# Kernel tuning notes

Measured on AMD Instinct MI355X. Metric: run time of the kernel, lower is better.

Reference implementation:

```python
import jax, jax.numpy as jnp
import numpy as np

NUM_EXPERTS = 2
HIDDEN = 768
BATCH = 32
SEQ = 2048
BALANCE_COEF = 0.01
LN_EPS = 1e-5


def setup_inputs() -> dict:
    key = jax.random.key(0)
    k1, k2, k3 = jax.random.split(key, 3)
    scale_in = 1.0
    scale_w = 1.0 / np.sqrt(HIDDEN)
    return {
        "inputs": jax.random.normal(k1, (BATCH, SEQ, HIDDEN), dtype=jnp.float32) * scale_in,
        "ln_gamma": jnp.ones((HIDDEN,), dtype=jnp.float32),
        "ln_beta": jnp.zeros((HIDDEN,), dtype=jnp.float32),
        "router_w": jax.random.normal(k2, (HIDDEN, NUM_EXPERTS), dtype=jnp.float32) * scale_w,
        "router_b": jnp.zeros((NUM_EXPERTS,), dtype=jnp.float32),
        "expert_w": jax.random.normal(k3, (NUM_EXPERTS, HIDDEN, HIDDEN), dtype=jnp.float32) * scale_w,
        "expert_b": jnp.zeros((NUM_EXPERTS, HIDDEN), dtype=jnp.float32),
    }


def _layer_norm(x, gamma, beta):
    mu = jnp.mean(x, axis=-1, keepdims=True)
    var = jnp.var(x, axis=-1, keepdims=True)
    return (x - mu) * jax.lax.rsqrt(var + LN_EPS) * gamma + beta


def reference(inputs, ln_gamma, ln_beta, router_w, router_b, expert_w, expert_b):
    # ---- router: mean-pool -> LayerNorm -> Linear -> softmax -> argmax ----
    seq_repr = jnp.mean(inputs, axis=1)                      # [B, H]
    seq_repr = _layer_norm(seq_repr, ln_gamma, ln_beta)      # [B, H]
    logits = seq_repr @ router_w + router_b                  # [B, E]
    probs = jax.nn.softmax(logits, axis=-1)                  # [B, E]
    expert_idx = jnp.argmax(probs, axis=-1)                  # [B]

    # ---- dispatch: each sequence goes to exactly one expert ----
    # Expert e: GELU(x @ W_e + b_e). Compute both, combine with one-hot mask
    # (jit-friendly equivalent of boolean-mask gather/scatter in the original).
    y = jnp.einsum('bsh,ehd->ebsd', inputs, expert_w) + expert_b[:, None, None, :]
    y = jax.nn.gelu(y)                                        # [E, B, S, H]
    one_hot = jax.nn.one_hot(expert_idx, NUM_EXPERTS, dtype=inputs.dtype)  # [B, E]
    output = jnp.einsum('ebsd,be->bsd', y, one_hot)           # [B, S, H]

    # ---- load-balancing loss: MSE(avg_probs, uniform) ----
    avg_probs = jnp.mean(probs, axis=0)                       # [E]
    balance_loss = jnp.mean((avg_probs - 1.0 / NUM_EXPERTS) ** 2)
    aux_loss = BALANCE_COEF * balance_loss  # experts contribute 0 aux here

    return output, aux_loss
```

## Files before the change

### kernel.cpp

```cpp
#include <hip/hip_runtime.h>
#include <hip/hip_bf16.h>
#include <stdint.h>

#define B_ 32
#define S_ 2048
#define H_ 768
#define E_ 2

typedef float f32x4 __attribute__((ext_vector_type(4)));
typedef short bf16x8 __attribute__((ext_vector_type(8)));

typedef const __attribute__((address_space(1))) void* gas_cvptr;
typedef __attribute__((address_space(3))) void* las_vptr;

__device__ __forceinline__ unsigned short f2bf(float f) {
    union { float f; uint32_t u; } v; v.f = f;
    uint32_t r = v.u + 0x7fffu + ((v.u >> 16) & 1u);
    return (unsigned short)(r >> 16);
}

__global__ __launch_bounds__(192) void convert_reduce(
    const float* __restrict__ in, unsigned short* __restrict__ xbf,
    float* __restrict__ seq_sum)
{
    const int b  = blockIdx.x >> 6;
    const int sc = blockIdx.x & 63;
    const int t  = threadIdx.x;
    float sx = 0.f, sy = 0.f, sz = 0.f, sw = 0.f;
    const int s0 = sc * 32;
#pragma unroll 4
    for (int s = s0; s < s0 + 32; ++s) {
        size_t ro = ((size_t)b * S_ + s) * (H_ / 4) + t;
        float4 v = ((const float4*)in)[ro];
        sx += v.x; sy += v.y; sz += v.z; sw += v.w;
        ushort4 o;
        o.x = f2bf(v.x); o.y = f2bf(v.y); o.z = f2bf(v.z); o.w = f2bf(v.w);
        ((ushort4*)xbf)[ro] = o;
    }
    float* dst = seq_sum + b * H_ + t * 4;
    atomicAdd(dst + 0, sx);
    atomicAdd(dst + 1, sy);
    atomicAdd(dst + 2, sz);
    atomicAdd(dst + 3, sw);
}

__global__ __launch_bounds__(256) void transpose_w(
    const float* __restrict__ w, unsigned short* __restrict__ wt)
{
    __shared__ float tile[64][65];
    const int tn = blockIdx.x, tk = blockIdx.y, e = blockIdx.z;
    const int t = threadIdx.x;
    const float* wb = w + (size_t)e * H_ * H_;
#pragma unroll
    for (int j = 0; j < 16; ++j) {
        int idx = j * 256 + t;
        int r = idx >> 6, c = idx & 63;
        tile[r][c] = wb[(size_t)(tk * 64 + r) * H_ + tn * 64 + c];
    }
    __syncthreads();
    unsigned short* wtb = wt + (size_t)e * H_ * H_;
#pragma unroll
    for (int j = 0; j < 16; ++j) {
        int idx = j * 256 + t;
        int r = idx >> 6, c = idx & 63;
        wtb[(size_t)(tn * 64 + r) * H_ + tk * 64 + c] = f2bf(tile[c][r]);
    }
}

__global__ __launch_bounds__(256) void router_kernel(
    const float* __restrict__ seq_sum, const float* __restrict__ gamma,
    const float* __restrict__ beta, const float* __restrict__ rw,
    const float* __restrict__ rb, int* __restrict__ eidx, float* __restrict__ psum)
{
    const int b = blockIdx.x;
    const int t = threadIdx.x;
    const int wave = t >> 6, lane = t & 63;
    __shared__ float red[8];
    float x[3];
    float s1 = 0.f, s2 = 0.f;
#pragma unroll
    for (int c = 0; c < 3; ++c) {
        int h = t + c * 256;
        float v = seq_sum[b * H_ + h] * (1.0f / (float)S_);
        x[c] = v; s1 += v; s2 += v * v;
    }
#pragma unroll
    for (int off = 32; off > 0; off >>= 1) {
        s1 += __shfl_down(s1, off, 64);
        s2 += __shfl_down(s2, off, 64);
    }
    if (lane == 0) { red[wave] = s1; red[4 + wave] = s2; }
    __syncthreads();
    s1 = red[0] + red[1] + red[2] + red[3];
    s2 = red[4] + red[5] + red[6] + red[7];
    const float mu = s1 * (1.0f / (float)H_);
    const float var = s2 * (1.0f / (float)H_) - mu * mu;
    const float rstd = rsqrtf(var + 1e-5f);
    float l0 = 0.f, l1 = 0.f;
#pragma unroll
    for (int c = 0; c < 3; ++c) {
        int h = t + c * 256;
        float nrm = (x[c] - mu) * rstd * gamma[h] + beta[h];
        l0 += nrm * rw[h * 2 + 0];
        l1 += nrm * rw[h * 2 + 1];
    }
    __syncthreads();
#pragma unroll
    for (int off = 32; off > 0; off >>= 1) {
        l0 += __shfl_down(l0, off, 64);
        l1 += __shfl_down(l1, off, 64);
    }
    if (lane == 0) { red[wave] = l0; red[4 + wave] = l1; }
    __syncthreads();
    if (t == 0) {
        l0 = red[0] + red[1] + red[2] + red[3] + rb[0];
        l1 = red[4] + red[5] + red[6] + red[7] + rb[1];
        float m = fmaxf(l0, l1);
        float p0 = expf(l0 - m), p1 = expf(l1 - m);
        float z = p0 + p1; p0 /= z; p1 /= z;
        eidx[b] = (l1 > l0) ? 1 : 0;
        atomicAdd(&psum[0], p0);
        atomicAdd(&psum[1], p1);
    }
}

__global__ void aux_kernel(const float* __restrict__ psum, float* __restrict__ out_aux)
{
    float a0 = psum[0] * (1.0f / (float)B_) - 0.5f;
    float a1 = psum[1] * (1.0f / (float)B_) - 0.5f;
    out_aux[0] = 0.01f * 0.5f * (a0 * a0 + a1 * a1);
}

__global__ __launch_bounds__(256) void moe_gemm(
    const unsigned short* __restrict__ xbf, const unsigned short* __restrict__ wt,
    const float* __restrict__ eb, const int* __restrict__ eidx,
    float* __restrict__ out)
{
    const int bn = blockIdx.x;
    const int bm = blockIdx.y;
    const int b  = blockIdx.z;
    const int tid  = threadIdx.x;
    const int wave = tid >> 6;
    const int lane = tid & 63;
    const int e = eidx[b];

    const unsigned short* Abase = xbf + (size_t)b * S_ * H_;
    const unsigned short* Bbase = wt  + (size_t)e * H_ * H_;

    __shared__ unsigned short lds_A[128 * 64];
    __shared__ unsigned short lds_B[128 * 64];

    f32x4 acc[4][4];
#pragma unroll
    for (int i = 0; i < 4; ++i)
#pragma unroll
        for (int j = 0; j < 4; ++j)
            acc[i][j] = (f32x4){0.f, 0.f, 0.f, 0.f};

    const int wm = (wave & 1) * 64;
    const int wn = (wave >> 1) * 64;
    const int rin = lane >> 3;
    const int chk = lane & 7;
    const int schk = chk ^ rin;

    for (int kt = 0; kt < H_ / 64; ++kt) {
        const int kb = kt * 64;
#pragma unroll
        for (int li = 0; li < 4; ++li) {
            const int i = wave * 4 + li;
            const int rA = bm * 128 + i * 8 + rin;
            const unsigned short* ga = Abase + (size_t)rA * H_ + kb + schk * 8;
            __builtin_amdgcn_global_load_lds((gas_cvptr)ga,
                (las_vptr)(lds_A + i * 512 + lane * 8), 16, 0, 0);
            const int rB = bn * 128 + i * 8 + rin;
            const unsigned short* gb = Bbase + (size_t)rB * H_ + kb + schk * 8;
            __builtin_amdgcn_global_load_lds((gas_cvptr)gb,
                (las_vptr)(lds_B + i * 512 + lane * 8), 16, 0, 0);
        }
        __syncthreads();
#pragma unroll
        for (int ks = 0; ks < 2; ++ks) {
            bf16x8 af[4], bfr[4];
#pragma unroll
            for (int i = 0; i < 4; ++i) {
                const int p = ((ks * 4 + (lane >> 4)) ^ (lane & 7));
                const int m = wm + i * 16 + (lane & 15);
                af[i] = *(const bf16x8*)(lds_A + m * 64 + p * 8);
                const int n = wn + i * 16 + (lane & 15);
                bfr[i] = *(const bf16x8*)(lds_B + n * 64 + p * 8);
            }
#pragma unroll
            for (int i = 0; i < 4; ++i)
#pragma unroll
                for (int j = 0; j < 4; ++j)
                    acc[i][j] = __builtin_amdgcn_mfma_f32_16x16x32_bf16(
                        af[i], bfr[j], acc[i][j], 0, 0, 0);
        }
        __syncthreads();
    }

    const int quad = lane >> 4;
    const int cn = lane & 15;
    float* outb = out + (size_t)b * S_ * H_;
#pragma unroll
    for (int i = 0; i < 4; ++i) {
#pragma unroll
        for (int j = 0; j < 4; ++j) {
            const int n = bn * 128 + wn + j * 16 + cn;
            const float bias = eb[e * H_ + n];
#pragma unroll
            for (int r = 0; r < 4; ++r) {
                const int m = bm * 128 + wm + i * 16 + quad * 4 + r;
                float v = acc[i][j][r] + bias;
                float u = 0.7978845608028654f * (v + 0.044715f * v * v * v);
                float th = 1.0f - 2.0f / (__expf(2.0f * u) + 1.0f);
                outb[(size_t)m * H_ + n] = 0.5f * v * (1.0f + th);
            }
        }
    }
}

extern "C" void kernel_launch(void* const* d_in, const int* in_sizes, int n_in,
                              void* d_out, int out_size, void* d_ws, size_t ws_size,
                              hipStream_t stream) {
    const float* inp   = (const float*)d_in[0];
    const float* gamma = (const float*)d_in[1];
    const float* beta  = (const float*)d_in[2];
    const float* rw    = (const float*)d_in[3];
    const float* rb    = (const float*)d_in[4];
    const float* ew    = (const float*)d_in[5];
    const float* eb    = (const float*)d_in[6];
    float* out = (float*)d_out;

    char* ws = (char*)d_ws;
    const size_t xbf_bytes = (size_t)B_ * S_ * H_ * 2;
    const size_t wt_bytes  = (size_t)E_ * H_ * H_ * 2;
    unsigned short* xbf = (unsigned short*)ws;
    unsigned short* wt  = (unsigned short*)(ws + xbf_bytes);
    float* seq_sum = (float*)(ws + xbf_bytes + wt_bytes);
    int*   eidx    = (int*)((char*)seq_sum + (size_t)B_ * H_ * 4);
    float* psum    = (float*)((char*)eidx + 128);

    hipMemsetAsync(seq_sum, 0, (size_t)B_ * H_ * 4 + 128 + 16, stream);

    convert_reduce<<<B_ * 64, 192, 0, stream>>>(inp, xbf, seq_sum);
    transpose_w<<<dim3(12, 12, E_), 256, 0, stream>>>(ew, wt);
    router_kernel<<<B_, 256, 0, stream>>>(seq_sum, gamma, beta, rw, rb, eidx, psum);
    aux_kernel<<<1, 1, 0, stream>>>(psum, out + (size_t)out_size - 1);
    moe_gemm<<<dim3(H_ / 128, S_ / 128, B_), 256, 0, stream>>>(xbf, wt, eb, eidx, out);
}
```

Before: 506.3 us.

## Double-buffer GEMM LDS tiles, swizzle block order, fuse aux into GEMM

Stages the next K tile into a second LDS buffer while the current one is consumed, using explicit vmcnt waits and barriers instead of a load-sync-compute-sync loop. The grid is flattened to 1D with an interleaved block-to-tile mapping, and launch_bounds is raised to request two blocks per SIMD. The aux-loss kernel is folded into the GEMM to save a launch. The GELU epilogue is rewritten as v*sigmoid(...) using a fast reciprocal, with bias hoisted out of the loop. The cost is doubled LDS use, which may limit occupancy, plus fragile hand-written waitcnt ordering.

```diff
diff --git a/kernel.cpp b/kernel.cpp
--- a/kernel.cpp
+++ b/kernel.cpp
@@ -124,31 +124,35 @@
     }
 }
 
-__global__ void aux_kernel(const float* __restrict__ psum, float* __restrict__ out_aux)
-{
-    float a0 = psum[0] * (1.0f / (float)B_) - 0.5f;
-    float a1 = psum[1] * (1.0f / (float)B_) - 0.5f;
-    out_aux[0] = 0.01f * 0.5f * (a0 * a0 + a1 * a1);
-}
-
-__global__ __launch_bounds__(256) void moe_gemm(
+__global__ __launch_bounds__(256, 2) void moe_gemm(
     const unsigned short* __restrict__ xbf, const unsigned short* __restrict__ wt,
     const float* __restrict__ eb, const int* __restrict__ eidx,
-    float* __restrict__ out)
-{
-    const int bn = blockIdx.x;
-    const int bm = blockIdx.y;
-    const int b  = blockIdx.z;
+    const float* __restrict__ psum, float* __restrict__ out,
+    float* __restrict__ out_aux)
+{
+    const int h    = blockIdx.x;
+    const int slot = (h >> 3) + (h & 7) * 384;
+    const int b    = slot / 96;
+    const int rr   = slot - b * 96;
+    const int bm   = rr / 6;
+    const int bn   = rr - bm * 6;
+
     const int tid  = threadIdx.x;
     const int wave = tid >> 6;
     const int lane = tid & 63;
     const int e = eidx[b];
 
+    if (h == 0 && tid == 0) {
+        float a0 = psum[0] * (1.0f / (float)B_) - 0.5f;
+        float a1 = psum[1] * (1.0f / (float)B_) - 0.5f;
+        out_aux[0] = 0.01f * 0.5f * (a0 * a0 + a1 * a1);
+    }
+
     const unsigned short* Abase = xbf + (size_t)b * S_ * H_;
     const unsigned short* Bbase = wt  + (size_t)e * H_ * H_;
 
-    __shared__ unsigned short lds_A[128 * 64];
-    __shared__ unsigned short lds_B[128 * 64];
+    __shared__ unsigned short lds_A[2][128 * 64];
+    __shared__ unsigned short lds_B[2][128 * 64];
 
     f32x4 acc[4][4];
 #pragma unroll
@@ -163,31 +167,30 @@
     const int chk = lane & 7;
     const int schk = chk ^ rin;
 
-    for (int kt = 0; kt < H_ / 64; ++kt) {
-        const int kb = kt * 64;
+    auto stage = [&](unsigned short* dA, unsigned short* dB, int kb) {
 #pragma unroll
         for (int li = 0; li < 4; ++li) {
             const int i = wave * 4 + li;
-            const int rA = bm * 128 + i * 8 + rin;
-            const unsigned short* ga = Abase + (size_t)rA * H_ + kb + schk * 8;
+            const unsigned short* ga = Abase + (size_t)(bm * 128 + i * 8 + rin) * H_ + kb + schk * 8;
             __builtin_amdgcn_global_load_lds((gas_cvptr)ga,
-                (las_vptr)(lds_A + i * 512 + lane * 8), 16, 0, 0);
-            const int rB = bn * 128 + i * 8 + rin;
-            const unsigned short* gb = Bbase + (size_t)rB * H_ + kb + schk * 8;
+                (las_vptr)(dA + i * 512 + lane * 8), 16, 0, 0);
+            const unsigned short* gb = Bbase + (size_t)(bn * 128 + i * 8 + rin) * H_ + kb + schk * 8;
             __builtin_amdgcn_global_load_lds((gas_cvptr)gb,
-                (las_vptr)(lds_B + i * 512 + lane * 8), 16, 0, 0);
-        }
-        __syncthreads();
+                (las_vptr)(dB + i * 512 + lane * 8), 16, 0, 0);
+        }
+    };
+
+    auto compute = [&](const unsigned short* LA, const unsigned short* LB) {
 #pragma unroll
         for (int ks = 0; ks < 2; ++ks) {
             bf16x8 af[4], bfr[4];
+            const int p = ((ks * 4 + (lane >> 4)) ^ (lane & 7));
 #pragma unroll
             for (int i = 0; i < 4; ++i) {
-                const int p = ((ks * 4 + (lane >> 4)) ^ (lane & 7));
                 const int m = wm + i * 16 + (lane & 15);
-                af[i] = *(const bf16x8*)(lds_A + m * 64 + p * 8);
+                af[i] = *(const bf16x8*)(LA + m * 64 + p * 8);
                 const int n = wn + i * 16 + (lane & 15);
-                bfr[i] = *(const bf16x8*)(lds_B + n * 64 + p * 8);
+                bfr[i] = *(const bf16x8*)(LB + n * 64 + p * 8);
             }
 #pragma unroll
             for (int i = 0; i < 4; ++i)
@@ -196,25 +199,50 @@
                     acc[i][j] = __builtin_amdgcn_mfma_f32_16x16x32_bf16(
                         af[i], bfr[j], acc[i][j], 0, 0, 0);
         }
-        __syncthreads();
+    };
+
+    stage(lds_A[0], lds_B[0], 0);
+#pragma unroll 1
+    for (int kt = 0; kt < 12; kt += 2) {
+        stage(lds_A[1], lds_B[1], (kt + 1) * 64);
+        asm volatile("s_waitcnt vmcnt(8)" ::: "memory");
+        __builtin_amdgcn_s_barrier();
+        asm volatile("" ::: "memory");
+        compute(lds_A[0], lds_B[0]);
+        __builtin_amdgcn_s_barrier();
+        asm volatile("" ::: "memory");
+        if (kt + 2 < 12) {
+            stage(lds_A[0], lds_B[0], (kt + 2) * 64);
+            asm volatile("s_waitcnt vmcnt(8)" ::: "memory");
+        } else {
+            asm volatile("s_waitcnt vmcnt(0)" ::: "memory");
+        }
+        __builtin_amdgcn_s_barrier();
+        asm volatile("" ::: "memory");
+        compute(lds_A[1], lds_B[1]);
+        __builtin_amdgcn_s_barrier();
+        asm volatile("" ::: "memory");
     }
 
     const int quad = lane >> 4;
     const int cn = lane & 15;
     float* outb = out + (size_t)b * S_ * H_;
+    float biasj[4];
+#pragma unroll
+    for (int j = 0; j < 4; ++j)
+        biasj[j] = eb[e * H_ + bn * 128 + wn + j * 16 + cn];
 #pragma unroll
     for (int i = 0; i < 4; ++i) {
-#pragma unroll
-        for (int j = 0; j < 4; ++j) {
-            const int n = bn * 128 + wn + j * 16 + cn;
-            const float bias = eb[e * H_ + n];
-#pragma unroll
-            for (int r = 0; r < 4; ++r) {
-                const int m = bm * 128 + wm + i * 16 + quad * 4 + r;
-                float v = acc[i][j][r] + bias;
-                float u = 0.7978845608028654f * (v + 0.044715f * v * v * v);
-                float th = 1.0f - 2.0f / (__expf(2.0f * u) + 1.0f);
-                outb[(size_t)m * H_ + n] = 0.5f * v * (1.0f + th);
+        const int m0 = bm * 128 + wm + i * 16 + quad * 4;
+#pragma unroll
+        for (int r = 0; r < 4; ++r) {
+            float* rowp = outb + (size_t)(m0 + r) * H_ + bn * 128 + wn + cn;
+#pragma unroll
+            for (int j = 0; j < 4; ++j) {
+                float v = acc[i][j][r] + biasj[j];
+                float u = -1.5957691216057308f * v - 0.07135481627362234f * (v * v * v);
+                float s = __builtin_amdgcn_rcpf(1.0f + __expf(u));
+                rowp[j * 16] = v * s;
             }
         }
     }
@@ -246,6 +274,6 @@
     convert_reduce<<<B_ * 64, 192, 0, stream>>>(inp, xbf, seq_sum);
     transpose_w<<<dim3(12, 12, E_), 256, 0, stream>>>(ew, wt);
     router_kernel<<<B_, 256, 0, stream>>>(seq_sum, gamma, beta, rw, rb, eidx, psum);
-    aux_kernel<<<1, 1, 0, stream>>>(psum, out + (size_t)out_size - 1);
-    moe_gemm<<<dim3(H_ / 128, S_ / 128, B_), 256, 0, stream>>>(xbf, wt, eb, eidx, out);
-}
+    moe_gemm<<<3072, 256, 0, stream>>>(xbf, wt, eb, eidx, psum, out,
+                                       out + (size_t)out_size - 1);
+}
```

After: 488.4 us. -3.5%, faster.
